# Performance work log

Measured on AMD Instinct MI355X. Metric: run time of the kernel, lower is better.

The kernel has to match this reference:

```python
import jax, jax.numpy as jnp
import numpy as np

STRIDE = 15           # cfg.shm.dilation_kernel
PAD = STRIDE // 2
P = 1048576           # cfg.shm.max_n_pixel (static sparse-pixel budget)


def dilate(alpha):
    # mask = (0.01 < alpha < 0.99); then 15x15 max-pool, stride 1, pad 7 (same size)
    m = jnp.logical_and(alpha > 0.01, alpha < 0.99).astype(alpha.dtype)
    return jax.lax.reduce_window(
        m, -jnp.inf, jax.lax.max,
        (1, 1, STRIDE, STRIDE), (1, 1, 1, 1),
        [(0, 0), (0, 0), (PAD, PAD), (PAD, PAD)])


def setup_inputs() -> dict:
    key = jax.random.key(0)
    ks = jax.random.split(key, 8)
    d = 128
    return {
        'image': jax.random.normal(ks[0], (8, 3, 512, 512), jnp.float32),
        'lr_pred': jax.random.uniform(ks[1], (8, 1, 512, 512), jnp.float32),
        'W1': jax.random.normal(ks[2], (4, d), jnp.float32) * 0.5,
        'b1': jnp.zeros((d,), jnp.float32),
        'W2': jax.random.normal(ks[3], (d, d), jnp.float32) * (1.0 / np.sqrt(d)),
        'b2': jnp.zeros((d,), jnp.float32),
        'W3': jax.random.normal(ks[4], (d, 1), jnp.float32) * (1.0 / np.sqrt(d)),
        'b3': jnp.zeros((1,), jnp.float32),
    }


def reference(image, lr_pred, W1, b1, W2, b2, W3, b3):
    B, C, H, W = image.shape
    mask = dilate(lr_pred)                       # [B,1,H,W] dilated uncertainty mask

    # generate_sparse_inputs: cat(img, (lr_pred-0.5)/0.5) channels-last, gather where mask>0
    feat = jnp.concatenate([image, (lr_pred - 0.5) / 0.5], axis=1)  # [B,4,H,W]
    feat = feat.transpose(0, 2, 3, 1).reshape(-1, C + 1)            # [B*H*W, 4]
    mflat = mask.reshape(-1)                                        # [B*H*W]

    (idx,) = jnp.nonzero(mflat > 0, size=P, fill_value=0)           # static-size gather
    count = jnp.sum(mflat > 0)
    valid = (jnp.arange(P) < count).astype(feat.dtype)              # [P]

    # torch's generate_sparse_inputs runs under no_grad -> stop_gradient on gather
    x = jax.lax.stop_gradient(feat[idx])                            # [P,4]

    # stand-in sparse head (shm): per-pixel MLP with sigmoid alpha output
    h = jax.nn.relu(x @ W1 + b1)
    h = jax.nn.relu(h @ W2 + b2)
    pred = jax.nn.sigmoid(h @ W3 + b3)[:, 0]                        # [P]

    # scatter predictions back to dense grid; ungathered masked pixels keep lr_pred
    scattered = jnp.zeros_like(mflat).at[idx].add(pred * valid)
    covered = jnp.zeros_like(mflat).at[idx].add(valid)
    lrf = lr_pred.reshape(-1)
    dense = scattered + (1.0 - covered) * lrf

    # final blend: pred*mask + lr_pred*(1-mask)
    final = dense * mflat + lrf * (1.0 - mflat)
    return final.reshape(B, 1, H, W)
```

## Files before the change

### kernel.cpp

```cpp
#include <hip/hip_runtime.h>
#include <math.h>

#define BB 8
#define HH 512
#define WW 512
#define NPIX (BB * HH * WW)
#define HWPIX (HH * WW)
#define PBUD 1048576
#define RAD 7
#define NB (NPIX / 256)
#define NMLP (NPIX / 128)

typedef __attribute__((ext_vector_type(4))) float f32x4;
typedef __attribute__((ext_vector_type(8))) short short8;

__device__ __forceinline__ unsigned short f2bf(float f) {
    unsigned int u = __float_as_uint(f);
    unsigned int r = (u + 0x7fffu + ((u >> 16) & 1u)) >> 16;
    return (unsigned short)r;
}

__global__ void k_prep_w2(const float* __restrict__ w2, unsigned short* __restrict__ w2f) {
    int i = blockIdx.x * 256 + threadIdx.x;
    int e  = i & 7;
    int l  = (i >> 3) & 63;
    int ks = (i >> 9) & 3;
    int jc = i >> 11;
    int j = jc * 16 + (l & 15);
    int k = ks * 32 + ((l >> 4) & 3) * 8 + e;
    w2f[i] = f2bf(w2[k * 128 + j]);
}

__global__ void k_rowdil(const float* __restrict__ lr, unsigned char* __restrict__ rowdil) {
    int p = blockIdx.x * 256 + threadIdx.x;
    int w = p & (WW - 1);
    int row0 = p - w;
    int lo = w - RAD; if (lo < 0) lo = 0;
    int hi = w + RAD; if (hi > WW - 1) hi = WW - 1;
    unsigned char any = 0;
    for (int x = lo; x <= hi; ++x) {
        float v = lr[row0 + x];
        any |= (unsigned char)(v > 0.01f && v < 0.99f);
    }
    rowdil[p] = any;
}

__global__ void k_coldil(const unsigned char* __restrict__ rowdil,
                         unsigned char* __restrict__ dm,
                         unsigned char* __restrict__ rankb,
                         int* __restrict__ gsum) {
    int p = blockIdx.x * 256 + threadIdx.x;
    int h = (p >> 9) & (HH - 1);
    int lo = h - RAD; if (lo < 0) lo = 0;
    int hi = h + RAD; if (hi > HH - 1) hi = HH - 1;
    lo -= h; hi -= h;
    unsigned char any = 0;
    for (int d = lo; d <= hi; ++d) any |= rowdil[p + d * WW];
    dm[p] = any;

    unsigned long long bal = __ballot(any != 0);
    __shared__ int wsum[4];
    int lane = threadIdx.x & 63;
    int wid  = threadIdx.x >> 6;
    if (lane == 0) wsum[wid] = __popcll(bal);
    __syncthreads();
    int pre = __popcll(bal & ((1ull << lane) - 1ull));
    int woff = 0;
    for (int i = 0; i < wid; ++i) woff += wsum[i];
    rankb[p] = (unsigned char)(woff + pre);
    if (threadIdx.x == 0) gsum[blockIdx.x] = wsum[0] + wsum[1] + wsum[2] + wsum[3];
}

__global__ void k_scan(const int* __restrict__ gsum, int* __restrict__ goff) {
    __shared__ int tsum[1024];
    int t = threadIdx.x;
    int base = t * 8;
    int v[8];
    int s = 0;
#pragma unroll
    for (int i = 0; i < 8; ++i) { v[i] = gsum[base + i]; s += v[i]; }
    tsum[t] = s;
    __syncthreads();
    for (int off = 1; off < 1024; off <<= 1) {
        int x = tsum[t];
        int y = (t >= off) ? tsum[t - off] : 0;
        __syncthreads();
        tsum[t] = x + y;
        __syncthreads();
    }
    int run = (t == 0) ? 0 : tsum[t - 1];
#pragma unroll
    for (int i = 0; i < 8; ++i) { goff[base + i] = run; run += v[i]; }
}

__global__ __launch_bounds__(256, 3)
void k_mlp(const float* __restrict__ image, const float* __restrict__ lr,
           const float* __restrict__ w1, const float* __restrict__ b1,
           const unsigned short* __restrict__ w2f, const float* __restrict__ b2,
           const float* __restrict__ w3, const float* __restrict__ b3,
           const unsigned char* __restrict__ dm, const unsigned char* __restrict__ rankb,
           const int* __restrict__ goff, float* __restrict__ out) {
    __shared__ __align__(16) char lds[32768];
    __shared__ int s_any;
    int g  = blockIdx.x;
    int p0 = g * 128;
    int t  = threadIdx.x;

    if (t == 0) s_any = 0;
    __syncthreads();
    if (t < 128) {
        int p = p0 + t;
        if (dm[p] && (goff[p >> 8] + (int)rankb[p] < PBUD)) s_any = 1;
    }
    __syncthreads();
    if (!s_any) {
        if (t < 128) out[p0 + t] = lr[p0 + t];
        return;
    }

    {
        int px = t & 127;
        int jh = __builtin_amdgcn_readfirstlane(t >> 7);
        int p  = p0 + px;
        float lrv = lr[p];
        size_t bimg = (size_t)(p >> 18) * 3 * HWPIX + (p & (HWPIX - 1));
        float x0 = image[bimg];
        float x1 = image[bimg + HWPIX];
        float x2 = image[bimg + 2 * HWPIX];
        float x3 = 2.0f * lrv - 1.0f;
#pragma unroll
        for (int jc8 = 0; jc8 < 8; ++jc8) {
            int jc = jh * 8 + jc8;
            unsigned short hv[8];
#pragma unroll
            for (int e = 0; e < 8; ++e) {
                int j = jc * 8 + e;
                float a = b1[j];
                a = fmaf(x0, w1[j], a);
                a = fmaf(x1, w1[128 + j], a);
                a = fmaf(x2, w1[256 + j], a);
                a = fmaf(x3, w1[384 + j], a);
                hv[e] = f2bf(fmaxf(a, 0.0f));
            }
            short8 pk;
#pragma unroll
            for (int e = 0; e < 8; ++e) pk[e] = (short)hv[e];
            int a = (((px << 8) | (jc << 4))) ^ ((px & 15) << 4);
            *(short8*)(lds + a) = pk;
        }
    }
    __syncthreads();

    int w    = t >> 6;
    int l    = t & 63;
    int lr16 = l & 15;
    int lh   = l >> 4;
    int rowbase = w * 32;

    short8 af[2][4];
#pragma unroll
    for (int ks = 0; ks < 4; ++ks) {
#pragma unroll
        for (int mt = 0; mt < 2; ++mt) {
            int row = rowbase + mt * 16 + lr16;
            int a = (((row << 8) | (ks << 6) | (lh << 4))) ^ ((row & 15) << 4);
            af[mt][ks] = *(const short8*)(lds + a);
        }
    }

    f32x4 acc[2][8];
#pragma unroll
    for (int mt = 0; mt < 2; ++mt)
#pragma unroll
        for (int jc = 0; jc < 8; ++jc) acc[mt][jc] = (f32x4){0.f, 0.f, 0.f, 0.f};

    const short8* wf = (const short8*)w2f;
#pragma unroll
    for (int jc = 0; jc < 8; ++jc) {
        short8 bf[4];
#pragma unroll
        for (int ks = 0; ks < 4; ++ks) bf[ks] = wf[(jc * 4 + ks) * 64 + l];
#pragma unroll
        for (int ks = 0; ks < 4; ++ks) {
            acc[0][jc] = __builtin_amdgcn_mfma_f32_16x16x32_bf16(af[0][ks], bf[ks], acc[0][jc], 0, 0, 0);
            acc[1][jc] = __builtin_amdgcn_mfma_f32_16x16x32_bf16(af[1][ks], bf[ks], acc[1][jc], 0, 0, 0);
        }
    }

    float b2v[8], w3v[8];
#pragma unroll
    for (int jc = 0; jc < 8; ++jc) {
        int col = jc * 16 + lr16;
        b2v[jc] = b2[col];
        w3v[jc] = w3[col];
    }
    float b3v = b3[0];

#pragma unroll
    for (int mt = 0; mt < 2; ++mt) {
#pragma unroll
        for (int r = 0; r < 4; ++r) {
            int row = rowbase + mt * 16 + lh * 4 + r;
            float part = 0.f;
#pragma unroll
            for (int jc = 0; jc < 8; ++jc)
                part += fmaxf(acc[mt][jc][r] + b2v[jc], 0.f) * w3v[jc];
            part += __shfl_xor(part, 1);
            part += __shfl_xor(part, 2);
            part += __shfl_xor(part, 4);
            part += __shfl_xor(part, 8);
            if (lr16 == 0) {
                int p = p0 + row;
                float lrv = lr[p];
                bool s = dm[p] && (goff[p >> 8] + (int)rankb[p] < PBUD);
                float logit = b3v + part;
                out[p] = s ? (1.0f / (1.0f + __expf(-logit))) : lrv;
            }
        }
    }
}

extern "C" void kernel_launch(void* const* d_in, const int* in_sizes, int n_in,
                              void* d_out, int out_size, void* d_ws, size_t ws_size,
                              hipStream_t stream) {
    const float* image = (const float*)d_in[0];
    const float* lr    = (const float*)d_in[1];
    const float* w1    = (const float*)d_in[2];
    const float* b1    = (const float*)d_in[3];
    const float* w2    = (const float*)d_in[4];
    const float* b2    = (const float*)d_in[5];
    const float* w3    = (const float*)d_in[6];
    const float* b3    = (const float*)d_in[7];
    float* out = (float*)d_out;

    char* ws = (char*)d_ws;
    unsigned char* rowdil = (unsigned char*)ws;
    unsigned char* dm     = (unsigned char*)(ws + (size_t)NPIX);
    unsigned char* rankb  = (unsigned char*)(ws + 2 * (size_t)NPIX);
    int* gsum             = (int*)(ws + 3 * (size_t)NPIX);
    int* goff             = (int*)(ws + 3 * (size_t)NPIX + NB * 4);
    unsigned short* w2f   = (unsigned short*)(ws + 3 * (size_t)NPIX + 2 * NB * 4);

    k_prep_w2<<<64, 256, 0, stream>>>(w2, w2f);
    k_rowdil <<<NPIX / 256, 256, 0, stream>>>(lr, rowdil);
    k_coldil <<<NB, 256, 0, stream>>>(rowdil, dm, rankb, gsum);
    k_scan   <<<1, 1024, 0, stream>>>(gsum, goff);
    k_mlp    <<<NMLP, 256, 0, stream>>>(image, lr, w1, b1, w2f, b2, w3, b3,
                                        dm, rankb, goff, out);
}
```

Measured before the change: 135.3 us.

## Compute first MLP layer with bf16 MFMA and fold biases into accumulators

The first layer (4->128 plus bias) moves from per-thread scalar FMAs to MFMA. The prep kernel packs W1 and b1 into a bf16 fragment layout padded to K=32, and pixel features are staged in LDS with a constant-1 column for the bias. Each wave then runs 16x16x32 MFMAs and writes the ReLU'd bf16 hidden activations into the swizzled LDS tile. The second-layer bias is preloaded into the accumulators, and the lr load is reused for the early-exit path. This removes many scalar FMAs and bf16 conversions, at the cost of extra LDS, an extra sync, and bf16 rounding of the inputs and W1.

```diff
diff --git a/kernel.cpp b/kernel.cpp
--- a/kernel.cpp
+++ b/kernel.cpp
@@ -1,4 +1,5 @@
 #include <hip/hip_runtime.h>
+#include <hip/hip_bf16.h>
 #include <math.h>
 
 #define BB 8
@@ -13,6 +14,8 @@
 
 typedef __attribute__((ext_vector_type(4))) float f32x4;
 typedef __attribute__((ext_vector_type(8))) short short8;
+typedef __attribute__((ext_vector_type(2))) unsigned int u32x2;
+typedef __attribute__((ext_vector_type(4))) unsigned int u32x4;
 
 __device__ __forceinline__ unsigned short f2bf(float f) {
     unsigned int u = __float_as_uint(f);
@@ -20,15 +23,33 @@
     return (unsigned short)r;
 }
 
-__global__ void k_prep_w2(const float* __restrict__ w2, unsigned short* __restrict__ w2f) {
+__device__ __forceinline__ unsigned int pkbf(float a, float b) {
+    __hip_bfloat162 h = __float22bfloat162_rn(make_float2(a, b));
+    return *(unsigned int*)&h;
+}
+
+__global__ void k_prep(const float* __restrict__ w2, const float* __restrict__ w1,
+                       const float* __restrict__ b1,
+                       unsigned short* __restrict__ w2f, unsigned short* __restrict__ w1f) {
     int i = blockIdx.x * 256 + threadIdx.x;
-    int e  = i & 7;
-    int l  = (i >> 3) & 63;
-    int ks = (i >> 9) & 3;
-    int jc = i >> 11;
-    int j = jc * 16 + (l & 15);
-    int k = ks * 32 + ((l >> 4) & 3) * 8 + e;
-    w2f[i] = f2bf(w2[k * 128 + j]);
+    if (i < 16384) {
+        int e  = i & 7;
+        int l  = (i >> 3) & 63;
+        int ks = (i >> 9) & 3;
+        int jc = i >> 11;
+        int j = jc * 16 + (l & 15);
+        int k = ks * 32 + ((l >> 4) & 3) * 8 + e;
+        w2f[i] = f2bf(w2[k * 128 + j]);
+    } else {
+        int i2 = i - 16384;
+        int e  = i2 & 7;
+        int l  = (i2 >> 3) & 63;
+        int fi = i2 >> 9;
+        int j = fi * 16 + (l & 15);
+        int k = ((l >> 4) & 3) * 8 + e;
+        float v = (k < 4) ? w1[k * 128 + j] : ((k == 4) ? b1[j] : 0.0f);
+        w1f[i2] = f2bf(v);
+    }
 }
 
 __global__ void k_rowdil(const float* __restrict__ lr, unsigned char* __restrict__ rowdil) {
@@ -95,12 +116,12 @@
 
 __global__ __launch_bounds__(256, 3)
 void k_mlp(const float* __restrict__ image, const float* __restrict__ lr,
-           const float* __restrict__ w1, const float* __restrict__ b1,
-           const unsigned short* __restrict__ w2f, const float* __restrict__ b2,
-           const float* __restrict__ w3, const float* __restrict__ b3,
+           const unsigned short* __restrict__ w1f, const unsigned short* __restrict__ w2f,
+           const float* __restrict__ b2, const float* __restrict__ w3,
+           const float* __restrict__ b3,
            const unsigned char* __restrict__ dm, const unsigned char* __restrict__ rankb,
            const int* __restrict__ goff, float* __restrict__ out) {
-    __shared__ __align__(16) char lds[32768];
+    __shared__ __align__(16) char lds[43008];
     __shared__ int s_any;
     int g  = blockIdx.x;
     int p0 = g * 128;
@@ -108,55 +129,70 @@
 
     if (t == 0) s_any = 0;
     __syncthreads();
+    float lrv0 = 0.f;
     if (t < 128) {
         int p = p0 + t;
+        lrv0 = lr[p];
         if (dm[p] && (goff[p >> 8] + (int)rankb[p] < PBUD)) s_any = 1;
     }
     __syncthreads();
     if (!s_any) {
-        if (t < 128) out[p0 + t] = lr[p0 + t];
+        if (t < 128) out[p0 + t] = lrv0;
         return;
     }
 
-    {
-        int px = t & 127;
-        int jh = __builtin_amdgcn_readfirstlane(t >> 7);
-        int p  = p0 + px;
-        float lrv = lr[p];
+    if (t < 128) {
+        int p = p0 + t;
         size_t bimg = (size_t)(p >> 18) * 3 * HWPIX + (p & (HWPIX - 1));
         float x0 = image[bimg];
         float x1 = image[bimg + HWPIX];
         float x2 = image[bimg + 2 * HWPIX];
-        float x3 = 2.0f * lrv - 1.0f;
-#pragma unroll
-        for (int jc8 = 0; jc8 < 8; ++jc8) {
-            int jc = jh * 8 + jc8;
-            unsigned short hv[8];
-#pragma unroll
-            for (int e = 0; e < 8; ++e) {
-                int j = jc * 8 + e;
-                float a = b1[j];
-                a = fmaf(x0, w1[j], a);
-                a = fmaf(x1, w1[128 + j], a);
-                a = fmaf(x2, w1[256 + j], a);
-                a = fmaf(x3, w1[384 + j], a);
-                hv[e] = f2bf(fmaxf(a, 0.0f));
-            }
-            short8 pk;
-#pragma unroll
-            for (int e = 0; e < 8; ++e) pk[e] = (short)hv[e];
-            int a = (((px << 8) | (jc << 4))) ^ ((px & 15) << 4);
-            *(short8*)(lds + a) = pk;
-        }
-    }
-    __syncthreads();
+        float x3 = 2.0f * lrv0 - 1.0f;
+        char* xr = lds + 32768 + t * 80;
+        u32x4 d0 = { pkbf(x0, x1), pkbf(x2, x3), pkbf(1.0f, 0.0f), 0u };
+        u32x4 z  = { 0u, 0u, 0u, 0u };
+        *(u32x4*)(xr)      = d0;
+        *(u32x4*)(xr + 16) = z;
+        *(u32x4*)(xr + 32) = z;
+        *(u32x4*)(xr + 48) = z;
+        *(u32x4*)(xr + 64) = z;
+    }
 
     int w    = t >> 6;
     int l    = t & 63;
     int lr16 = l & 15;
-    int lh   = l >> 4;
+    int lh   = (l >> 4) & 3;
+
+    const short8* wf1 = (const short8*)w1f;
+    short8 a1_0 = wf1[(w * 2 + 0) * 64 + l];
+    short8 a1_1 = wf1[(w * 2 + 1) * 64 + l];
+    __syncthreads();
+
+#pragma unroll
+    for (int jc = 0; jc < 8; ++jc) {
+        int px = jc * 16 + lr16;
+        short8 xb = *(const short8*)(lds + 32768 + px * 80 + lh * 16);
+        f32x4 c0 = {0.f, 0.f, 0.f, 0.f};
+        f32x4 c1 = {0.f, 0.f, 0.f, 0.f};
+        c0 = __builtin_amdgcn_mfma_f32_16x16x32_bf16(a1_0, xb, c0, 0, 0, 0);
+        c1 = __builtin_amdgcn_mfma_f32_16x16x32_bf16(a1_1, xb, c1, 0, 0, 0);
+        int swz = (px & 15) << 4;
+        {
+            int j0 = (w * 2 + 0) * 16 + lh * 4;
+            u32x2 u = { pkbf(fmaxf(c0[0], 0.f), fmaxf(c0[1], 0.f)),
+                        pkbf(fmaxf(c0[2], 0.f), fmaxf(c0[3], 0.f)) };
+            *(u32x2*)(lds + (((px << 8) | (j0 << 1)) ^ swz)) = u;
+        }
+        {
+            int j1 = (w * 2 + 1) * 16 + lh * 4;
+            u32x2 u = { pkbf(fmaxf(c1[0], 0.f), fmaxf(c1[1], 0.f)),
+                        pkbf(fmaxf(c1[2], 0.f), fmaxf(c1[3], 0.f)) };
+            *(u32x2*)(lds + (((px << 8) | (j1 << 1)) ^ swz)) = u;
+        }
+    }
+    __syncthreads();
+
     int rowbase = w * 32;
-
     short8 af[2][4];
 #pragma unroll
     for (int ks = 0; ks < 4; ++ks) {
@@ -168,25 +204,6 @@
         }
     }
 
-    f32x4 acc[2][8];
-#pragma unroll
-    for (int mt = 0; mt < 2; ++mt)
-#pragma unroll
-        for (int jc = 0; jc < 8; ++jc) acc[mt][jc] = (f32x4){0.f, 0.f, 0.f, 0.f};
-
-    const short8* wf = (const short8*)w2f;
-#pragma unroll
-    for (int jc = 0; jc < 8; ++jc) {
-        short8 bf[4];
-#pragma unroll
-        for (int ks = 0; ks < 4; ++ks) bf[ks] = wf[(jc * 4 + ks) * 64 + l];
-#pragma unroll
-        for (int ks = 0; ks < 4; ++ks) {
-            acc[0][jc] = __builtin_amdgcn_mfma_f32_16x16x32_bf16(af[0][ks], bf[ks], acc[0][jc], 0, 0, 0);
-            acc[1][jc] = __builtin_amdgcn_mfma_f32_16x16x32_bf16(af[1][ks], bf[ks], acc[1][jc], 0, 0, 0);
-        }
-    }
-
     float b2v[8], w3v[8];
 #pragma unroll
     for (int jc = 0; jc < 8; ++jc) {
@@ -196,6 +213,26 @@
     }
     float b3v = b3[0];
 
+    f32x4 acc[2][8];
+#pragma unroll
+    for (int mt = 0; mt < 2; ++mt)
+#pragma unroll
+        for (int jc = 0; jc < 8; ++jc)
+            acc[mt][jc] = (f32x4){b2v[jc], b2v[jc], b2v[jc], b2v[jc]};
+
+    const short8* wf = (const short8*)w2f;
+#pragma unroll
+    for (int jc = 0; jc < 8; ++jc) {
+        short8 bf[4];
+#pragma unroll
+        for (int ks = 0; ks < 4; ++ks) bf[ks] = wf[(jc * 4 + ks) * 64 + l];
+#pragma unroll
+        for (int ks = 0; ks < 4; ++ks) {
+            acc[0][jc] = __builtin_amdgcn_mfma_f32_16x16x32_bf16(af[0][ks], bf[ks], acc[0][jc], 0, 0, 0);
+            acc[1][jc] = __builtin_amdgcn_mfma_f32_16x16x32_bf16(af[1][ks], bf[ks], acc[1][jc], 0, 0, 0);
+        }
+    }
+
 #pragma unroll
     for (int mt = 0; mt < 2; ++mt) {
 #pragma unroll
@@ -204,7 +241,7 @@
             float part = 0.f;
 #pragma unroll
             for (int jc = 0; jc < 8; ++jc)
-                part += fmaxf(acc[mt][jc][r] + b2v[jc], 0.f) * w3v[jc];
+                part += fmaxf(acc[mt][jc][r], 0.f) * w3v[jc];
             part += __shfl_xor(part, 1);
             part += __shfl_xor(part, 2);
             part += __shfl_xor(part, 4);
@@ -240,11 +277,12 @@
     int* gsum             = (int*)(ws + 3 * (size_t)NPIX);
     int* goff             = (int*)(ws + 3 * (size_t)NPIX + NB * 4);
     unsigned short* w2f   = (unsigned short*)(ws + 3 * (size_t)NPIX + 2 * NB * 4);
-
-    k_prep_w2<<<64, 256, 0, stream>>>(w2, w2f);
-    k_rowdil <<<NPIX / 256, 256, 0, stream>>>(lr, rowdil);
-    k_coldil <<<NB, 256, 0, stream>>>(rowdil, dm, rankb, gsum);
-    k_scan   <<<1, 1024, 0, stream>>>(gsum, goff);
-    k_mlp    <<<NMLP, 256, 0, stream>>>(image, lr, w1, b1, w2f, b2, w3, b3,
-                                        dm, rankb, goff, out);
-}
+    unsigned short* w1f   = w2f + 16384;
+
+    k_prep  <<<80, 256, 0, stream>>>(w2, w1, b1, w2f, w1f);
+    k_rowdil<<<NPIX / 256, 256, 0, stream>>>(lr, rowdil);
+    k_coldil<<<NB, 256, 0, stream>>>(rowdil, dm, rankb, gsum);
+    k_scan  <<<1, 1024, 0, stream>>>(gsum, goff);
+    k_mlp   <<<NMLP, 256, 0, stream>>>(image, lr, w1f, w2f, b2, w3, b3,
+                                       dm, rankb, goff, out);
+}
```

Result: slower. 152.3 us (+12.5%).
